# Kernel tuning notes

Hardware: AMD Instinct MI355X
Metric: run time of the kernel (lower is better)

The kernel has to match this reference:

```python
import jax, jax.numpy as jnp
import numpy as np

B, N, M, K = 8, 8192, 512, 32
C_IN, EMB = 3, 256
RADIUS2 = 0.1 * 0.1
EPS = 1e-5


def setup_inputs() -> dict:
    key = jax.random.key(0)
    ks = jax.random.split(key, 8)
    p = jax.random.uniform(ks[0], (B, N, 3), dtype=jnp.float32)           # coords in [0,1]^3
    x = jax.random.normal(ks[1], (B, C_IN, N), dtype=jnp.float32)          # features [B,C,N]
    def w(k, co, ci):
        return jax.random.normal(k, (co, ci), dtype=jnp.float32) / np.float32(np.sqrt(ci))
    return {
        "p": p, "x": x,
        # conv1: (6->256, BN+ReLU), (256->256, plain+bias)
        "W0": w(ks[2], EMB, 6), "g0": jnp.ones((EMB,), jnp.float32), "be0": jnp.zeros((EMB,), jnp.float32),
        "W1": w(ks[3], EMB, EMB), "b1": jnp.zeros((EMB,), jnp.float32),
        # conv2 (input doubled to 512): (512->512, BN+ReLU), (512->256, plain+bias)
        "W2": w(ks[4], 2 * EMB, 2 * EMB), "g2": jnp.ones((2 * EMB,), jnp.float32), "be2": jnp.zeros((2 * EMB,), jnp.float32),
        "W3": w(ks[5], EMB, 2 * EMB), "b3": jnp.zeros((EMB,), jnp.float32),
    }


def furthest_point_sample(p, m):
    # p: [B,N,3] -> idx [B,m] int32; starts at index 0 (matches CUDA FPS)
    b, n, _ = p.shape
    def step(carry, _):
        min_d, last = carry
        last_pt = jnp.take_along_axis(p, last[:, None, None], axis=1)     # [B,1,3]
        d = jnp.sum((p - last_pt) ** 2, axis=-1)                           # [B,N]
        min_d = jnp.minimum(min_d, d)
        nxt = jnp.argmax(min_d, axis=-1).astype(jnp.int32)
        return (min_d, nxt), last
    init = (jnp.full((b, n), 1e10, p.dtype), jnp.zeros((b,), jnp.int32))
    _, idx = jax.lax.scan(step, init, None, length=m)
    return idx.T                                                           # [B,m]


def ball_query(center_p, p, k, r2):
    # first-k-in-order points within radius; pad with first valid (center is always valid)
    d2 = jnp.sum((center_p[:, :, None, :] - p[:, None, :, :]) ** 2, axis=-1)  # [B,M,N]
    n = p.shape[1]
    keyv = jnp.where(d2 < r2, jnp.arange(n, dtype=jnp.int32), jnp.int32(n))   # [B,M,N]
    keys = jnp.sort(keyv, axis=-1)[..., :k]                                    # [B,M,K]
    valid = keys < n
    idx = jnp.where(valid, keys, keys[..., 0:1])
    return idx.astype(jnp.int32)


def bn_relu(f, g, b):
    # training-mode BatchNorm2d over (B, M, K) per channel, then ReLU
    mu = jnp.mean(f, axis=(0, 2, 3), keepdims=True)
    var = jnp.var(f, axis=(0, 2, 3), keepdims=True)
    fh = (f - mu) * jax.lax.rsqrt(var + EPS)
    return jax.nn.relu(fh * g[None, :, None, None] + b[None, :, None, None])


def reference(p, x, W0, g0, be0, W1, b1, W2, g2, be2, W3, b3):
    idx = furthest_point_sample(p, M)                                       # [B,M]
    center_p = jnp.take_along_axis(p, idx[:, :, None], axis=1)              # [B,M,3]
    gidx = ball_query(center_p, p, K, RADIUS2)                              # [B,M,K]
    grouped_xyz = jax.vmap(lambda pts, ix: pts[ix])(p, gidx)                # [B,M,K,3]
    dp = jnp.transpose(grouped_xyz - center_p[:, :, None, :], (0, 3, 1, 2))  # [B,3,M,K]
    fj = jax.vmap(lambda ft, ix: ft[:, ix])(x, gidx)                        # [B,C,M,K]
    center_x = jnp.take_along_axis(x, idx[:, None, :], axis=2)              # [B,C,M]
    f = jnp.concatenate([dp, fj - center_x[..., None]], axis=1)             # [B,6,M,K]  (dp_df)
    # conv1
    f = bn_relu(jnp.einsum('oc,bcmk->bomk', W0, f), g0, be0)
    f = jnp.einsum('oc,bcmk->bomk', W1, f) + b1[None, :, None, None]
    # mid max-pool concat
    fmax = jnp.max(f, axis=-1, keepdims=True)
    f = jnp.concatenate([jnp.broadcast_to(fmax, f.shape), f], axis=1)       # [B,512,M,K]
    # conv2
    f = bn_relu(jnp.einsum('oc,bcmk->bomk', W2, f), g2, be2)
    f = jnp.einsum('oc,bcmk->bomk', W3, f) + b3[None, :, None, None]
    out_f = jnp.max(f, axis=-1)                                             # [B,256,M]
    return (p, center_p, x, out_f)
```

## Files before the change

kernel.cpp:

```cpp
#include <hip/hip_runtime.h>

typedef unsigned short u16;
typedef unsigned int u32;
typedef unsigned long long u64;
typedef __bf16 bf16x8 __attribute__((ext_vector_type(8)));
typedef float v4f32 __attribute__((ext_vector_type(4)));

#define NP 8192
#define NM 512
#define LTOT 131072
#define NBM 4096
#define R2F 0.009999999776482582f

__device__ __forceinline__ float bf2f(u16 u) { return __uint_as_float(((u32)u) << 16); }
__device__ __forceinline__ u16 f2bf(float f) {
  u32 u = __float_as_uint(f);
  return (u16)((u + 0x7fffu + ((u >> 16) & 1u)) >> 16);
}
__device__ __forceinline__ void gl16(const void* g, void* l) {
  __builtin_amdgcn_global_load_lds((const __attribute__((address_space(1))) u32*)g,
                                   (__attribute__((address_space(3))) u32*)l, 16, 0, 0);
}

#define MFMA_COMPUTE() do { \
  bf16x8 a_[4], b_[4]; \
  _Pragma("unroll") \
  for (int mi_ = 0; mi_ < 4; ++mi_) a_[mi_] = *(const bf16x8*)&As[(wrow + mi_*16 + l15)*32 + l4*8]; \
  _Pragma("unroll") \
  for (int ni_ = 0; ni_ < 4; ++ni_) b_[ni_] = *(const bf16x8*)&Bs[(wcol + ni_*16 + l15)*32 + l4*8]; \
  _Pragma("unroll") \
  for (int mi_ = 0; mi_ < 4; ++mi_) { \
    _Pragma("unroll") \
    for (int ni_ = 0; ni_ < 4; ++ni_) \
      acc[mi_][ni_] = __builtin_amdgcn_mfma_f32_16x16x32_bf16(a_[mi_], b_[ni_], acc[mi_][ni_], 0, 0, 0); \
  } \
} while (0)

__global__ __launch_bounds__(1024) void k_fps_prep(
    const float* __restrict__ p, const float* __restrict__ x,
    const float* __restrict__ W1, const float* __restrict__ W2, const float* __restrict__ W3,
    float* __restrict__ outP, float* __restrict__ outC, float* __restrict__ outX,
    u16* __restrict__ w1b, u16* __restrict__ w2b, u16* __restrict__ w3b,
    float* __restrict__ statz, int* __restrict__ idxb)
{
  const int tid = threadIdx.x;
  if (blockIdx.x >= 8) {
    for (size_t i = (size_t)(blockIdx.x - 8) * 1024 + tid; i < 855040; i += 104 * 1024) {
      if (i < 196608)      outP[i] = p[i];
      else if (i < 393216) outX[i - 196608] = x[i - 196608];
      else if (i < 458752) w1b[i - 393216] = f2bf(W1[i - 393216]);
      else if (i < 720896) w2b[i - 458752] = f2bf(W2[i - 458752]);
      else if (i < 851968) w3b[i - 720896] = f2bf(W3[i - 720896]);
      else                 statz[i - 851968] = 0.0f;
    }
    return;
  }
  const int b = blockIdx.x;
  const float* pb = p + (size_t)b * NP * 3;
  __shared__ float pl[NP * 3];
  __shared__ u64 slot[3];
  float px[8], py[8], pz[8], md[8];
  u32 nj[8];
  #pragma unroll
  for (int q = 0; q < 8; ++q) {
    int j = tid + (q << 10);
    float a0 = pb[j*3+0], a1 = pb[j*3+1], a2 = pb[j*3+2];
    px[q] = a0; py[q] = a1; pz[q] = a2; md[q] = 1e10f;
    nj[q] = ~(u32)j;
    pl[j*3+0] = a0; pl[j*3+1] = a1; pl[j*3+2] = a2;
  }
  if (tid < 3) slot[tid] = 0ull;
  __syncthreads();
  int last = 0;
  float* ctr = outC + (size_t)b * NM * 3;
  int* ip = idxb + b * NM;
  for (int s = 0; s < NM; ++s) {
    const int sl = s % 3;
    float lx = pl[last*3], ly = pl[last*3+1], lz = pl[last*3+2];
    if (tid == 0) {
      ip[s] = last; ctr[s*3] = lx; ctr[s*3+1] = ly; ctr[s*3+2] = lz;
      slot[(s+1) % 3] = 0ull;
    }
    u64 bk = 0;
    #pragma unroll
    for (int q = 0; q < 8; ++q) {
      float dx = __fsub_rn(px[q], lx), dy = __fsub_rn(py[q], ly), dz = __fsub_rn(pz[q], lz);
      float d = __fadd_rn(__fadd_rn(__fmul_rn(dx,dx), __fmul_rn(dy,dy)), __fmul_rn(dz,dz));
      float nm = fminf(md[q], d);
      md[q] = nm;
      u64 key = ((u64)__float_as_uint(nm) << 32) | (u64)nj[q];
      bk = key > bk ? key : bk;
    }
    #pragma unroll
    for (int off = 1; off < 64; off <<= 1) {
      u64 o = __shfl_xor(bk, off);
      if (o > bk) bk = o;
    }
    if ((tid & 63) == 0)
      __hip_atomic_fetch_max(&slot[sl], bk, __ATOMIC_RELAXED, __HIP_MEMORY_SCOPE_WORKGROUP);
    __syncthreads();
    last = (int)(~(u32)(slot[sl] & 0xffffffffull));
  }
}

__global__ __launch_bounds__(256) void k_group(
    const float* __restrict__ p, const float* __restrict__ x,
    const float* __restrict__ ctr, const int* __restrict__ idxb,
    u16* __restrict__ f0)
{
  const int tid = threadIdx.x, wv = tid >> 6, lane = tid & 63;
  const int cm = blockIdx.x * 4 + wv;
  const int b = cm >> 9;
  __shared__ int selS[4][33];
  volatile int* sel = selS[wv];
  const float cx0 = ctr[cm*3+0], cy0 = ctr[cm*3+1], cz0 = ctr[cm*3+2];
  const float* pb = p + (size_t)b * NP * 3;
  int cnt = 0;
  for (int ch = 0; ch < NP/64; ++ch) {
    if (cnt >= 32) break;
    int j = (ch << 6) + lane;
    float qx = pb[j*3], qy = pb[j*3+1], qz = pb[j*3+2];
    float dx = __fsub_rn(cx0,qx), dy = __fsub_rn(cy0,qy), dz = __fsub_rn(cz0,qz);
    float d2 = __fadd_rn(__fadd_rn(__fmul_rn(dx,dx),__fmul_rn(dy,dy)),__fmul_rn(dz,dz));
    bool pr = d2 < R2F;
    u64 msk = __ballot(pr);
    int pos = cnt + (int)__popcll(msk & ((1ull << lane) - 1ull));
    if (pr && pos < 32) sel[pos] = j;
    cnt += (int)__popcll(msk);
  }
  if (lane < 32) {
    int jj = (lane < cnt) ? sel[lane] : sel[0];
    const float* xb = x + (size_t)b * 3 * NP;
    int ic = idxb[cm];
    float gx = pb[jj*3], gy = pb[jj*3+1], gz = pb[jj*3+2];
    size_t col = (size_t)cm * 32 + lane;
    f0[0*(size_t)LTOT + col] = f2bf(gx - cx0);
    f0[1*(size_t)LTOT + col] = f2bf(gy - cy0);
    f0[2*(size_t)LTOT + col] = f2bf(gz - cz0);
    f0[3*(size_t)LTOT + col] = f2bf(xb[jj]      - xb[ic]);
    f0[4*(size_t)LTOT + col] = f2bf(xb[NP+jj]   - xb[NP+ic]);
    f0[5*(size_t)LTOT + col] = f2bf(xb[2*NP+jj] - xb[2*NP+ic]);
  }
}

__global__ __launch_bounds__(256) void k_g1(
    const u16* __restrict__ f0, const float* __restrict__ W0, u16* __restrict__ h1)
{
  __shared__ float w0l[1536];
  const int tid = threadIdx.x;
  for (int i = tid; i < 1536; i += 256) w0l[i] = W0[i];
  __syncthreads();
  const size_t col = (size_t)blockIdx.x * 256 + tid;
  float fin[6];
  #pragma unroll
  for (int c = 0; c < 6; ++c) fin[c] = bf2f(f0[(size_t)c * LTOT + col]);
  #pragma unroll
  for (int ob = 0; ob < 8; ++ob) {
    u32 w[16];
    #pragma unroll
    for (int pr2 = 0; pr2 < 16; ++pr2) {
      float v0 = 0.f, v1 = 0.f;
      int o0 = ob*32 + pr2*2;
      #pragma unroll
      for (int c = 0; c < 6; ++c) {
        v0 = fmaf(w0l[o0*6 + c], fin[c], v0);
        v1 = fmaf(w0l[(o0+1)*6 + c], fin[c], v1);
      }
      w[pr2] = (u32)f2bf(v0) | ((u32)f2bf(v1) << 16);
    }
    uint4* dst = (uint4*)(h1 + ((size_t)ob * LTOT + col) * 32);
    #pragma unroll
    for (int t4 = 0; t4 < 4; ++t4)
      dst[t4] = make_uint4(w[t4*4], w[t4*4+1], w[t4*4+2], w[t4*4+3]);
  }
}

__global__ __launch_bounds__(256) void k_stat(
    const u16* __restrict__ hb, float* __restrict__ sums, float* __restrict__ sqs)
{
  const int tid = threadIdx.x;
  const int cb = blockIdx.x >> 5, cc = blockIdx.x & 31;
  const int slot = tid & 3, cl = tid >> 2;
  float s[8], q[8];
  #pragma unroll
  for (int j = 0; j < 8; ++j) { s[j] = 0.f; q[j] = 0.f; }
  const u16* base = hb + (size_t)cb * LTOT * 32;
  for (int i = 0; i < 64; ++i) {
    size_t col = (size_t)cc * 4096 + i * 64 + cl;
    uint4 v = *(const uint4*)(base + col * 32 + slot * 8);
    u32 qa[4] = {v.x, v.y, v.z, v.w};
    #pragma unroll
    for (int t2 = 0; t2 < 4; ++t2) {
      float lo = bf2f((u16)(qa[t2] & 0xffffu));
      float hi = bf2f((u16)(qa[t2] >> 16));
      s[2*t2]   += lo; q[2*t2]   = fmaf(lo, lo, q[2*t2]);
      s[2*t2+1] += hi; q[2*t2+1] = fmaf(hi, hi, q[2*t2+1]);
    }
  }
  __shared__ float ls[32], lq[32];
  if (tid < 32) { ls[tid] = 0.f; lq[tid] = 0.f; }
  __syncthreads();
  #pragma unroll
  for (int j = 0; j < 8; ++j) {
    atomicAdd(&ls[slot*8 + j], s[j]);
    atomicAdd(&lq[slot*8 + j], q[j]);
  }
  __syncthreads();
  if (tid < 32) {
    atomicAdd(&sums[cb*32 + tid], ls[tid]);
    atomicAdd(&sqs[cb*32 + tid], lq[tid]);
  }
}

__global__ void k_fin(const float* __restrict__ sums, const float* __restrict__ sqs,
                      const float* __restrict__ g, const float* __restrict__ be,
                      float* __restrict__ S, float* __restrict__ T, int C)
{
  int t = threadIdx.x;
  if (t < C) {
    const float inv = 1.0f / 131072.0f;
    float mu = sums[t] * inv;
    float var = sqs[t] * inv - mu * mu;
    float s = g[t] / sqrtf(var + 1e-5f);
    S[t] = s; T[t] = be[t] - mu * s;
  }
}

__device__ __forceinline__ void xf_store(u16* Bs, int idx, uint4 q, int cb,
                                         const float* sS, const float* sT)
{
  u32 w[4]; u32 qa[4] = {q.x, q.y, q.z, q.w};
  #pragma unroll
  for (int t2 = 0; t2 < 4; ++t2) {
    float a  = fmaxf(fmaf(sS[cb + 2*t2],     bf2f((u16)(qa[t2] & 0xffffu)), sT[cb + 2*t2]), 0.f);
    float bv = fmaxf(fmaf(sS[cb + 2*t2 + 1], bf2f((u16)(qa[t2] >> 16)),     sT[cb + 2*t2 + 1]), 0.f);
    w[t2] = (u32)f2bf(a) | ((u32)f2bf(bv) << 16);
  }
  *(uint4*)&Bs[idx * 8] = make_uint4(w[0], w[1], w[2], w[3]);
}

__global__ __launch_bounds__(256) void k_gemm2(
    const u16* __restrict__ wA, const u16* __restrict__ hin,
    const float* __restrict__ Sc, const float* __restrict__ Tc,
    const float* __restrict__ bias,
    u16* __restrict__ h2, u16* __restrict__ fmaxb)
{
  __shared__ alignas(16) u16 As[4096];
  __shared__ alignas(16) u16 Bs[4096];
  __shared__ float sS[256], sT[256];
  const int tid = threadIdx.x;
  sS[tid] = Sc[tid]; sT[tid] = Tc[tid];
  const int oT = blockIdx.x & 1, cT = blockIdx.x >> 1;
  const int lane = tid & 63, wv = tid >> 6;
  const int wrow = (wv >> 1) * 64, wcol = (wv & 1) * 64;
  const int l15 = lane & 15, l4 = lane >> 4;
  v4f32 acc[4][4];
  #pragma unroll
  for (int mi = 0; mi < 4; ++mi)
    #pragma unroll
    for (int ni = 0; ni < 4; ++ni) acc[mi][ni] = (v4f32){0.f,0.f,0.f,0.f};
  const int idx0 = tid, idx1 = 256 + tid;
  const int r0 = idx0 >> 2, sg0 = idx0 & 3, r1 = idx1 >> 2, sg1 = idx1 & 3;
  __syncthreads();
  for (int kt = 0; kt < 8; ++kt) {
    const size_t bb = (size_t)kt * LTOT + (size_t)cT * 128;
    uint4 q0 = *(const uint4*)(hin + (bb + r0) * 32 + sg0 * 8);
    uint4 q1 = *(const uint4*)(hin + (bb + r1) * 32 + sg1 * 8);
    if (kt) __syncthreads();
    gl16(wA + (size_t)(oT*128 + r0) * 256 + kt*32 + sg0*8, &As[idx0 * 8]);
    gl16(wA + (size_t)(oT*128 + r1) * 256 + kt*32 + sg1*8, &As[idx1 * 8]);
    xf_store(Bs, idx0, q0, kt*32 + sg0*8, sS, sT);
    xf_store(Bs, idx1, q1, kt*32 + sg1*8, sS, sT);
    asm volatile("s_waitcnt vmcnt(0)" ::: "memory");
    __syncthreads();
    MFMA_COMPUTE();
  }
  const int oB = oT*128 + wrow + l4*4;
  const int cB = cT*128 + wcol + l15;
  #pragma unroll
  for (int mi = 0; mi < 4; ++mi) {
    const float4 bv = *(const float4*)&bias[oB + mi*16];
    #pragma unroll
    for (int ni = 0; ni < 4; ++ni) {
      acc[mi][ni][0] += bv.x; acc[mi][ni][1] += bv.y;
      acc[mi][ni][2] += bv.z; acc[mi][ni][3] += bv.w;
    }
  }
  #pragma unroll
  for (int mi = 0; mi < 4; ++mi) {
    const int o = oB + mi*16;
    const size_t rb = (size_t)(o >> 5) * LTOT * 32 + (o & 31);
    #pragma unroll
    for (int ni = 0; ni < 4; ++ni) {
      ushort4 u; u.x = f2bf(acc[mi][ni][0]); u.y = f2bf(acc[mi][ni][1]);
      u.z = f2bf(acc[mi][ni][2]); u.w = f2bf(acc[mi][ni][3]);
      *(ushort4*)&h2[rb + (size_t)(cB + ni*16) * 32] = u;
    }
  }
  #pragma unroll
  for (int g = 0; g < 2; ++g) {
    const int bm = (cT*128 + wcol + g*32) >> 5;
    #pragma unroll
    for (int mi = 0; mi < 4; ++mi) {
      float a0 = fmaxf(acc[mi][2*g][0], acc[mi][2*g+1][0]);
      float a1 = fmaxf(acc[mi][2*g][1], acc[mi][2*g+1][1]);
      float a2 = fmaxf(acc[mi][2*g][2], acc[mi][2*g+1][2]);
      float a3 = fmaxf(acc[mi][2*g][3], acc[mi][2*g+1][3]);
      #pragma unroll
      for (int off = 1; off < 16; off <<= 1) {
        a0 = fmaxf(a0, __shfl_xor(a0, off));
        a1 = fmaxf(a1, __shfl_xor(a1, off));
        a2 = fmaxf(a2, __shfl_xor(a2, off));
        a3 = fmaxf(a3, __shfl_xor(a3, off));
      }
      if (l15 == 0) {
        const int o = oB + mi*16;
        ushort4 u; u.x=f2bf(a0); u.y=f2bf(a1); u.z=f2bf(a2); u.w=f2bf(a3);
        *(ushort4*)&fmaxb[((size_t)(o >> 5) * NBM + bm) * 32 + (o & 31)] = u;
      }
    }
  }
}

__global__ __launch_bounds__(256) void k_fmb(
    const u16* __restrict__ wA, const u16* __restrict__ fmaxb, float* __restrict__ fmb)
{
  __shared__ alignas(16) u16 As[4096];
  __shared__ alignas(16) u16 Bs[4096];
  const int tid = threadIdx.x;
  const int oT = blockIdx.x & 3, cT = blockIdx.x >> 2;
  const int lane = tid & 63, wv = tid >> 6;
  const int wrow = (wv >> 1) * 64, wcol = (wv & 1) * 64;
  const int l15 = lane & 15, l4 = lane >> 4;
  v4f32 acc[4][4];
  #pragma unroll
  for (int mi = 0; mi < 4; ++mi)
    #pragma unroll
    for (int ni = 0; ni < 4; ++ni) acc[mi][ni] = (v4f32){0.f,0.f,0.f,0.f};
  const int idx0 = tid, idx1 = 256 + tid;
  const int r0 = idx0 >> 2, sg0 = idx0 & 3, r1 = idx1 >> 2, sg1 = idx1 & 3;
  for (int kt = 0; kt < 8; ++kt) {
    if (kt) __syncthreads();
    gl16(wA + (size_t)(oT*128 + r0) * 512 + kt*32 + sg0*8, &As[idx0 * 8]);
    gl16(wA + (size_t)(oT*128 + r1) * 512 + kt*32 + sg1*8, &As[idx1 * 8]);
    const size_t bb = (size_t)kt * NBM + (size_t)cT * 128;
    gl16(fmaxb + (bb + r0) * 32 + sg0 * 8, &Bs[idx0 * 8]);
    gl16(fmaxb + (bb + r1) * 32 + sg1 * 8, &Bs[idx1 * 8]);
    asm volatile("s_waitcnt vmcnt(0)" ::: "memory");
    __syncthreads();
    MFMA_COMPUTE();
  }
  const int oB = oT*128 + wrow + l4*4;
  const int cB = cT*128 + wcol + l15;
  #pragma unroll
  for (int mi = 0; mi < 4; ++mi) {
    const int o = oB + mi*16;
    #pragma unroll
    for (int ni = 0; ni < 4; ++ni) {
      const int colg = cB + ni*16;
      fmb[(size_t)(o+0)*NBM + colg] = acc[mi][ni][0];
      fmb[(size_t)(o+1)*NBM + colg] = acc[mi][ni][1];
      fmb[(size_t)(o+2)*NBM + colg] = acc[mi][ni][2];
      fmb[(size_t)(o+3)*NBM + colg] = acc[mi][ni][3];
    }
  }
}

__global__ __launch_bounds__(256) void k_gemm3(
    const u16* __restrict__ wA, const u16* __restrict__ hin,
    const float* __restrict__ fmb, u16* __restrict__ h3)
{
  __shared__ alignas(16) u16 As[4096];
  __shared__ alignas(16) u16 Bs[4096];
  const int tid = threadIdx.x;
  const int oT = blockIdx.x & 3, cT = blockIdx.x >> 2;
  const int lane = tid & 63, wv = tid >> 6;
  const int wrow = (wv >> 1) * 64, wcol = (wv & 1) * 64;
  const int l15 = lane & 15, l4 = lane >> 4;
  v4f32 acc[4][4];
  #pragma unroll
  for (int mi = 0; mi < 4; ++mi)
    #pragma unroll
    for (int ni = 0; ni < 4; ++ni) acc[mi][ni] = (v4f32){0.f,0.f,0.f,0.f};
  const int idx0 = tid, idx1 = 256 + tid;
  const int r0 = idx0 >> 2, sg0 = idx0 & 3, r1 = idx1 >> 2, sg1 = idx1 & 3;
  for (int kt = 0; kt < 8; ++kt) {
    if (kt) __syncthreads();
    gl16(wA + (size_t)(oT*128 + r0) * 512 + 256 + kt*32 + sg0*8, &As[idx0 * 8]);
    gl16(wA + (size_t)(oT*128 + r1) * 512 + 256 + kt*32 + sg1*8, &As[idx1 * 8]);
    const size_t bb = (size_t)kt * LTOT + (size_t)cT * 128;
    gl16(hin + (bb + r0) * 32 + sg0 * 8, &Bs[idx0 * 8]);
    gl16(hin + (bb + r1) * 32 + sg1 * 8, &Bs[idx1 * 8]);
    asm volatile("s_waitcnt vmcnt(0)" ::: "memory");
    __syncthreads();
    MFMA_COMPUTE();
  }
  const int oB = oT*128 + wrow + l4*4;
  const int cB = cT*128 + wcol + l15;
  #pragma unroll
  for (int mi = 0; mi < 4; ++mi) {
    const int o = oB + mi*16;
    const size_t rb = (size_t)(o >> 5) * LTOT * 32 + (o & 31);
    #pragma unroll
    for (int hf = 0; hf < 2; ++hf) {
      const int bm = (cT*128 + wcol + hf*32) >> 5;
      float e0 = fmb[(size_t)(o+0)*NBM + bm];
      float e1 = fmb[(size_t)(o+1)*NBM + bm];
      float e2 = fmb[(size_t)(o+2)*NBM + bm];
      float e3 = fmb[(size_t)(o+3)*NBM + bm];
      #pragma unroll
      for (int nn = 0; nn < 2; ++nn) {
        const int ni = hf*2 + nn;
        ushort4 u;
        u.x = f2bf(acc[mi][ni][0] + e0);
        u.y = f2bf(acc[mi][ni][1] + e1);
        u.z = f2bf(acc[mi][ni][2] + e2);
        u.w = f2bf(acc[mi][ni][3] + e3);
        *(ushort4*)&h3[rb + (size_t)(cB + ni*16) * 32] = u;
      }
    }
  }
}

__global__ __launch_bounds__(256) void k_gemm4(
    const u16* __restrict__ wA, const u16* __restrict__ hin,
    const float* __restrict__ Sc, const float* __restrict__ Tc,
    const float* __restrict__ bias, float* __restrict__ outF)
{
  __shared__ alignas(16) u16 As[4096];
  __shared__ alignas(16) u16 Bs[4096];
  __shared__ float sS[512], sT[512];
  const int tid = threadIdx.x;
  sS[tid] = Sc[tid]; sT[tid] = Tc[tid];
  sS[tid+256] = Sc[tid+256]; sT[tid+256] = Tc[tid+256];
  const int oT = blockIdx.x & 1, cT = blockIdx.x >> 1;
  const int lane = tid & 63, wv = tid >> 6;
  const int wrow = (wv >> 1) * 64, wcol = (wv & 1) * 64;
  const int l15 = lane & 15, l4 = lane >> 4;
  v4f32 acc[4][4];
  #pragma unroll
  for (int mi = 0; mi < 4; ++mi)
    #pragma unroll
    for (int ni = 0; ni < 4; ++ni) acc[mi][ni] = (v4f32){0.f,0.f,0.f,0.f};
  const int idx0 = tid, idx1 = 256 + tid;
  const int r0 = idx0 >> 2, sg0 = idx0 & 3, r1 = idx1 >> 2, sg1 = idx1 & 3;
  __syncthreads();
  for (int kt = 0; kt < 16; ++kt) {
    const size_t bb = (size_t)kt * LTOT + (size_t)cT * 128;
    uint4 q0 = *(const uint4*)(hin + (bb + r0) * 32 + sg0 * 8);
    uint4 q1 = *(const uint4*)(hin + (bb + r1) * 32 + sg1 * 8);
    if (kt) __syncthreads();
    gl16(wA + (size_t)(oT*128 + r0) * 512 + kt*32 + sg0*8, &As[idx0 * 8]);
    gl16(wA + (size_t)(oT*128 + r1) * 512 + kt*32 + sg1*8, &As[idx1 * 8]);
    xf_store(Bs, idx0, q0, kt*32 + sg0*8, sS, sT);
    xf_store(Bs, idx1, q1, kt*32 + sg1*8, sS, sT);
    asm volatile("s_waitcnt vmcnt(0)" ::: "memory");
    __syncthreads();
    MFMA_COMPUTE();
  }
  const int oB = oT*128 + wrow + l4*4;
  #pragma unroll
  for (int mi = 0; mi < 4; ++mi) {
    const float4 bv = *(const float4*)&bias[oB + mi*16];
    #pragma unroll
    for (int ni = 0; ni < 4; ++ni) {
      acc[mi][ni][0] += bv.x; acc[mi][ni][1] += bv.y;
      acc[mi][ni][2] += bv.z; acc[mi][ni][3] += bv.w;
    }
  }
  #pragma unroll
  for (int g = 0; g < 2; ++g) {
    const int bm = (cT*128 + wcol + g*32) >> 5;
    const int bI = bm >> 9, mm = bm & 511;
    #pragma unroll
    for (int mi = 0; mi < 4; ++mi) {
      float a0 = fmaxf(acc[mi][2*g][0], acc[mi][2*g+1][0]);
      float a1 = fmaxf(acc[mi][2*g][1], acc[mi][2*g+1][1]);
      float a2 = fmaxf(acc[mi][2*g][2], acc[mi][2*g+1][2]);
      float a3 = fmaxf(acc[mi][2*g][3], acc[mi][2*g+1][3]);
      #pragma unroll
      for (int off = 1; off < 16; off <<= 1) {
        a0 = fmaxf(a0, __shfl_xor(a0, off));
        a1 = fmaxf(a1, __shfl_xor(a1, off));
        a2 = fmaxf(a2, __shfl_xor(a2, off));
        a3 = fmaxf(a3, __shfl_xor(a3, off));
      }
      if (l15 == 0) {
        const int o = oB + mi*16;
        outF[((size_t)bI*256 + o+0)*512 + mm] = a0;
        outF[((size_t)bI*256 + o+1)*512 + mm] = a1;
        outF[((size_t)bI*256 + o+2)*512 + mm] = a2;
        outF[((size_t)bI*256 + o+3)*512 + mm] = a3;
      }
    }
  }
}

extern "C" void kernel_launch(void* const* d_in, const int* in_sizes, int n_in,
                              void* d_out, int out_size, void* d_ws, size_t ws_size,
                              hipStream_t stream)
{
  (void)in_sizes; (void)n_in; (void)out_size; (void)ws_size;
  const float* p   = (const float*)d_in[0];
  const float* x   = (const float*)d_in[1];
  const float* W0  = (const float*)d_in[2];
  const float* g0  = (const float*)d_in[3];
  const float* be0 = (const float*)d_in[4];
  const float* W1  = (const float*)d_in[5];
  const float* b1  = (const float*)d_in[6];
  const float* W2  = (const float*)d_in[7];
  const float* g2  = (const float*)d_in[8];
  const float* be2 = (const float*)d_in[9];
  const float* W3  = (const float*)d_in[10];
  const float* b3  = (const float*)d_in[11];
  float* out  = (float*)d_out;
  float* outP = out;
  float* outC = out + 196608;
  float* outX = out + 208896;
  float* outF = out + 405504;
  char* ws = (char*)d_ws;
  u16* h2    = (u16*)(ws);
  u16* h3    = (u16*)(ws + 67108864);
  u16* h1    = h3;
  u16* f0    = (u16*)(ws + 201326592);
  u16* fmaxb = (u16*)(ws + 202899456);
  float* fmb = (float*)(ws + 204996608);
  u16* w1b   = (u16*)(ws + 213385216);
  u16* w2b   = (u16*)(ws + 213516288);
  u16* w3b   = (u16*)(ws + 214040576);
  int* idxb  = (int*)(ws + 214302720);
  float* statz = (float*)(ws + 214319104);
  float* sum1 = statz;        float* sq1 = statz + 256;
  float* sum2 = statz + 512;  float* sq2 = statz + 1024;
  float* s0 = statz + 1536;   float* t0 = statz + 1792;
  float* s2 = statz + 2048;   float* t2 = statz + 2560;

  k_fps_prep<<<112, 1024, 0, stream>>>(p, x, W1, W2, W3, outP, outC, outX,
                                       w1b, w2b, w3b, statz, idxb);
  k_group<<<1024, 256, 0, stream>>>(p, x, outC, idxb, f0);
  k_g1<<<512, 256, 0, stream>>>(f0, W0, h1);
  k_stat<<<256, 256, 0, stream>>>(h1, sum1, sq1);
  k_fin<<<1, 512, 0, stream>>>(sum1, sq1, g0, be0, s0, t0, 256);
  k_gemm2<<<2048, 256, 0, stream>>>(w1b, h1, s0, t0, b1, h2, fmaxb);
  k_fmb<<<128, 256, 0, stream>>>(w2b, fmaxb, fmb);
  k_gemm3<<<4096, 256, 0, stream>>>(w2b, h2, fmb, h3);
  k_stat<<<512, 256, 0, stream>>>(h3, sum2, sq2);
  k_fin<<<1, 512, 0, stream>>>(sum2, sq2, g2, be2, s2, t2, 512);
  k_gemm4<<<2048, 256, 0, stream>>>(w3b, h3, s2, t2, b3, outF);
}
```

Baseline: 905.9 us.

## Speed up FPS argmax with packed fp32 math and DPP float max plus ballot

The sequential furthest-point-sampling loop now computes distances with packed v_pk_add/v_pk_mul fp32 instructions, two points per instruction. The per-step argmax no longer runs a 64-bit key shuffle reduction. It does a 32-bit float max through DPP row/bcast steps, reads lane 63, and recovers the smallest matching index with ballots and ctz. This cuts the latency of the 512 serial steps, which bound the FPS block. It relies on float max equality and ballot ordering to keep the smallest-index tie-break, and replacing rounded fsub with adding a negated value keeps the arithmetic bit-exact.

```diff
diff --git a/kernel.cpp b/kernel.cpp
--- a/kernel.cpp
+++ b/kernel.cpp
@@ -5,6 +5,7 @@
 typedef unsigned long long u64;
 typedef __bf16 bf16x8 __attribute__((ext_vector_type(8)));
 typedef float v4f32 __attribute__((ext_vector_type(4)));
+typedef float f32x2 __attribute__((ext_vector_type(2)));
 
 #define NP 8192
 #define NM 512
@@ -20,6 +21,27 @@
 __device__ __forceinline__ void gl16(const void* g, void* l) {
   __builtin_amdgcn_global_load_lds((const __attribute__((address_space(1))) u32*)g,
                                    (__attribute__((address_space(3))) u32*)l, 16, 0, 0);
+}
+
+__device__ __forceinline__ f32x2 pk_add(f32x2 a, f32x2 b) {
+  f32x2 r; asm("v_pk_add_f32 %0, %1, %2" : "=v"(r) : "v"(a), "v"(b)); return r;
+}
+__device__ __forceinline__ f32x2 pk_mul(f32x2 a, f32x2 b) {
+  f32x2 r; asm("v_pk_mul_f32 %0, %1, %2" : "=v"(r) : "v"(a), "v"(b)); return r;
+}
+
+__device__ __forceinline__ float wave_fmax_dpp63(float v) {
+#define FSTEP(CTRL) { \
+    u32 o_ = (u32)__builtin_amdgcn_update_dpp(0, (int)__float_as_uint(v), CTRL, 0xF, 0xF, true); \
+    v = fmaxf(v, __uint_as_float(o_)); }
+  FSTEP(0x111)
+  FSTEP(0x112)
+  FSTEP(0x114)
+  FSTEP(0x118)
+  FSTEP(0x142)
+  FSTEP(0x143)
+#undef FSTEP
+  return v;
 }
 
 #define MFMA_COMPUTE() do { \
@@ -59,17 +81,17 @@
   const float* pb = p + (size_t)b * NP * 3;
   __shared__ float pl[NP * 3];
   __shared__ u64 slot[3];
-  float px[8], py[8], pz[8], md[8];
-  u32 nj[8];
+  f32x2 pxv[4], pyv[4], pzv[4];
+  float md[8];
   #pragma unroll
   for (int q = 0; q < 8; ++q) {
     int j = tid + (q << 10);
     float a0 = pb[j*3+0], a1 = pb[j*3+1], a2 = pb[j*3+2];
-    px[q] = a0; py[q] = a1; pz[q] = a2; md[q] = 1e10f;
-    nj[q] = ~(u32)j;
+    pxv[q>>1][q&1] = a0; pyv[q>>1][q&1] = a1; pzv[q>>1][q&1] = a2; md[q] = 1e10f;
     pl[j*3+0] = a0; pl[j*3+1] = a1; pl[j*3+2] = a2;
   }
   if (tid < 3) slot[tid] = 0ull;
+  const u32 wbase = (u32)__builtin_amdgcn_readfirstlane(tid & 0x3C0);
   __syncthreads();
   int last = 0;
   float* ctr = outC + (size_t)b * NM * 3;
@@ -81,23 +103,31 @@
       ip[s] = last; ctr[s*3] = lx; ctr[s*3+1] = ly; ctr[s*3+2] = lz;
       slot[(s+1) % 3] = 0ull;
     }
-    u64 bk = 0;
-    #pragma unroll
-    for (int q = 0; q < 8; ++q) {
-      float dx = __fsub_rn(px[q], lx), dy = __fsub_rn(py[q], ly), dz = __fsub_rn(pz[q], lz);
-      float d = __fadd_rn(__fadd_rn(__fmul_rn(dx,dx), __fmul_rn(dy,dy)), __fmul_rn(dz,dz));
-      float nm = fminf(md[q], d);
-      md[q] = nm;
-      u64 key = ((u64)__float_as_uint(nm) << 32) | (u64)nj[q];
-      bk = key > bk ? key : bk;
-    }
-    #pragma unroll
-    for (int off = 1; off < 64; off <<= 1) {
-      u64 o = __shfl_xor(bk, off);
-      if (o > bk) bk = o;
+    const f32x2 nlx = {-lx, -lx}, nly = {-ly, -ly}, nlz = {-lz, -lz};
+    #pragma unroll
+    for (int h = 0; h < 4; ++h) {
+      f32x2 dx = pk_add(pxv[h], nlx);
+      f32x2 dy = pk_add(pyv[h], nly);
+      f32x2 dz = pk_add(pzv[h], nlz);
+      f32x2 d2 = pk_add(pk_add(pk_mul(dx,dx), pk_mul(dy,dy)), pk_mul(dz,dz));
+      md[2*h]   = fminf(md[2*h],   d2.x);
+      md[2*h+1] = fminf(md[2*h+1], d2.y);
+    }
+    float t01 = fmaxf(md[0], md[1]), t23 = fmaxf(md[2], md[3]);
+    float t45 = fmaxf(md[4], md[5]), t67 = fmaxf(md[6], md[7]);
+    float wmx = fmaxf(fmaxf(t01, t23), fmaxf(t45, t67));
+    wmx = wave_fmax_dpp63(wmx);
+    u32 wmb = (u32)__builtin_amdgcn_readlane((int)__float_as_uint(wmx), 63);
+    float wm = __uint_as_float(wmb);
+    u32 jq = 0;
+    #pragma unroll
+    for (int q = 7; q >= 0; --q) {
+      u64 mq = __ballot(md[q] == wm);
+      if (mq) jq = (u32)__builtin_ctzll(mq) + (u32)(q << 10);
     }
     if ((tid & 63) == 0)
-      __hip_atomic_fetch_max(&slot[sl], bk, __ATOMIC_RELAXED, __HIP_MEMORY_SCOPE_WORKGROUP);
+      __hip_atomic_fetch_max(&slot[sl], ((u64)wmb << 32) | (u64)(~(wbase + jq)),
+                             __ATOMIC_RELAXED, __HIP_MEMORY_SCOPE_WORKGROUP);
     __syncthreads();
     last = (int)(~(u32)(slot[sl] & 0xffffffffull));
   }
```

After: 817.6 us. 9.7% less time.

## Derive first BN stats from input covariance, fuse second BN stats into GEMM epilogue

Applied to the files above, without the earlier changes.

The first BatchNorm statistics now come from a 6-channel input moment matrix (first and second moments), which k_fin1 projects through W0 analytically. This replaces the pass over the 256-channel h1 buffer. The second BN's sum and sum-of-squares are accumulated inside the k_gemm3 epilogue with wave shuffles and global atomics, which removes the separate k_stat read of h3. The trade-offs: the stats are taken from fp32 values rather than bf16-rounded ones, the covariance form can lose precision through cancellation, and the GEMM epilogue now issues many atomics.

```diff
diff --git a/kernel.cpp b/kernel.cpp
--- a/kernel.cpp
+++ b/kernel.cpp
@@ -143,6 +143,78 @@
   }
 }
 
+__global__ __launch_bounds__(256) void k_cov(const u16* __restrict__ f0, float* __restrict__ cov)
+{
+  const int tid = threadIdx.x;
+  const size_t col = (size_t)blockIdx.x * 256 + tid;
+  float f[6];
+  #pragma unroll
+  for (int c = 0; c < 6; ++c) f[c] = bf2f(f0[(size_t)c * LTOT + col]);
+  float v[27];
+  int n = 0;
+  #pragma unroll
+  for (int c = 0; c < 6; ++c) v[n++] = f[c];
+  #pragma unroll
+  for (int i = 0; i < 6; ++i)
+    #pragma unroll
+    for (int j = i; j < 6; ++j) v[n++] = f[i] * f[j];
+  #pragma unroll
+  for (int k = 0; k < 27; ++k) {
+    float s = v[k];
+    #pragma unroll
+    for (int off = 1; off < 64; off <<= 1) s += __shfl_xor(s, off);
+    v[k] = s;
+  }
+  __shared__ float ls[27];
+  if (tid < 27) ls[tid] = 0.f;
+  __syncthreads();
+  if ((tid & 63) == 0) {
+    #pragma unroll
+    for (int k = 0; k < 27; ++k) atomicAdd(&ls[k], v[k]);
+  }
+  __syncthreads();
+  if (tid < 27) atomicAdd(&cov[tid], ls[tid]);
+}
+
+__global__ void k_fin1(const float* __restrict__ cov, const float* __restrict__ W0,
+                       const float* __restrict__ g, const float* __restrict__ be,
+                       float* __restrict__ S, float* __restrict__ T)
+{
+  int c = threadIdx.x;
+  const float inv = 1.0f / 131072.0f;
+  float w[6];
+  #pragma unroll
+  for (int k = 0; k < 6; ++k) w[k] = W0[c*6 + k];
+  float mu = 0.f;
+  #pragma unroll
+  for (int k = 0; k < 6; ++k) mu = fmaf(w[k], cov[k], mu);
+  mu *= inv;
+  float e2 = 0.f;
+  int n = 6;
+  #pragma unroll
+  for (int i = 0; i < 6; ++i)
+    #pragma unroll
+    for (int j = i; j < 6; ++j) {
+      float coeff = (i == j) ? w[i]*w[j] : 2.f*w[i]*w[j];
+      e2 = fmaf(coeff, cov[n++] * inv, e2);
+    }
+  float var = e2 - mu * mu;
+  float s = g[c] / sqrtf(var + 1e-5f);
+  S[c] = s; T[c] = be[c] - mu * s;
+}
+
+__global__ void k_fin2(const float* __restrict__ sums, const float* __restrict__ sqs,
+                       const float* __restrict__ g, const float* __restrict__ be,
+                       float* __restrict__ S, float* __restrict__ T)
+{
+  int t = threadIdx.x;
+  const float inv = 1.0f / 131072.0f;
+  float mu = sums[t] * inv;
+  float var = sqs[t] * inv - mu * mu;
+  float s = g[t] / sqrtf(var + 1e-5f);
+  S[t] = s; T[t] = be[t] - mu * s;
+}
+
 __global__ __launch_bounds__(256) void k_g1(
     const u16* __restrict__ f0, const float* __restrict__ W0, u16* __restrict__ h1)
 {
@@ -172,57 +244,6 @@
     #pragma unroll
     for (int t4 = 0; t4 < 4; ++t4)
       dst[t4] = make_uint4(w[t4*4], w[t4*4+1], w[t4*4+2], w[t4*4+3]);
-  }
-}
-
-__global__ __launch_bounds__(256) void k_stat(
-    const u16* __restrict__ hb, float* __restrict__ sums, float* __restrict__ sqs)
-{
-  const int tid = threadIdx.x;
-  const int cb = blockIdx.x >> 5, cc = blockIdx.x & 31;
-  const int slot = tid & 3, cl = tid >> 2;
-  float s[8], q[8];
-  #pragma unroll
-  for (int j = 0; j < 8; ++j) { s[j] = 0.f; q[j] = 0.f; }
-  const u16* base = hb + (size_t)cb * LTOT * 32;
-  for (int i = 0; i < 64; ++i) {
-    size_t col = (size_t)cc * 4096 + i * 64 + cl;
-    uint4 v = *(const uint4*)(base + col * 32 + slot * 8);
-    u32 qa[4] = {v.x, v.y, v.z, v.w};
-    #pragma unroll
-    for (int t2 = 0; t2 < 4; ++t2) {
-      float lo = bf2f((u16)(qa[t2] & 0xffffu));
-      float hi = bf2f((u16)(qa[t2] >> 16));
-      s[2*t2]   += lo; q[2*t2]   = fmaf(lo, lo, q[2*t2]);
-      s[2*t2+1] += hi; q[2*t2+1] = fmaf(hi, hi, q[2*t2+1]);
-    }
-  }
-  __shared__ float ls[32], lq[32];
-  if (tid < 32) { ls[tid] = 0.f; lq[tid] = 0.f; }
-  __syncthreads();
-  #pragma unroll
-  for (int j = 0; j < 8; ++j) {
-    atomicAdd(&ls[slot*8 + j], s[j]);
-    atomicAdd(&lq[slot*8 + j], q[j]);
-  }
-  __syncthreads();
-  if (tid < 32) {
-    atomicAdd(&sums[cb*32 + tid], ls[tid]);
-    atomicAdd(&sqs[cb*32 + tid], lq[tid]);
-  }
-}
-
-__global__ void k_fin(const float* __restrict__ sums, const float* __restrict__ sqs,
-                      const float* __restrict__ g, const float* __restrict__ be,
-                      float* __restrict__ S, float* __restrict__ T, int C)
-{
-  int t = threadIdx.x;
-  if (t < C) {
-    const float inv = 1.0f / 131072.0f;
-    float mu = sums[t] * inv;
-    float var = sqs[t] * inv - mu * mu;
-    float s = g[t] / sqrtf(var + 1e-5f);
-    S[t] = s; T[t] = be[t] - mu * s;
   }
 }
 
@@ -368,7 +389,8 @@
 
 __global__ __launch_bounds__(256) void k_gemm3(
     const u16* __restrict__ wA, const u16* __restrict__ hin,
-    const float* __restrict__ fmb, u16* __restrict__ h3)
+    const float* __restrict__ fmb, u16* __restrict__ h3,
+    float* __restrict__ stS, float* __restrict__ stQ)
 {
   __shared__ alignas(16) u16 As[4096];
   __shared__ alignas(16) u16 Bs[4096];
@@ -401,6 +423,7 @@
   for (int mi = 0; mi < 4; ++mi) {
     const int o = oB + mi*16;
     const size_t rb = (size_t)(o >> 5) * LTOT * 32 + (o & 31);
+    float st[4] = {0.f,0.f,0.f,0.f}, sq[4] = {0.f,0.f,0.f,0.f};
     #pragma unroll
     for (int hf = 0; hf < 2; ++hf) {
       const int bm = (cT*128 + wcol + hf*32) >> 5;
@@ -411,12 +434,30 @@
       #pragma unroll
       for (int nn = 0; nn < 2; ++nn) {
         const int ni = hf*2 + nn;
+        float v0 = acc[mi][ni][0] + e0;
+        float v1 = acc[mi][ni][1] + e1;
+        float v2 = acc[mi][ni][2] + e2;
+        float v3 = acc[mi][ni][3] + e3;
+        st[0] += v0; sq[0] = fmaf(v0, v0, sq[0]);
+        st[1] += v1; sq[1] = fmaf(v1, v1, sq[1]);
+        st[2] += v2; sq[2] = fmaf(v2, v2, sq[2]);
+        st[3] += v3; sq[3] = fmaf(v3, v3, sq[3]);
         ushort4 u;
-        u.x = f2bf(acc[mi][ni][0] + e0);
-        u.y = f2bf(acc[mi][ni][1] + e1);
-        u.z = f2bf(acc[mi][ni][2] + e2);
-        u.w = f2bf(acc[mi][ni][3] + e3);
+        u.x = f2bf(v0); u.y = f2bf(v1); u.z = f2bf(v2); u.w = f2bf(v3);
         *(ushort4*)&h3[rb + (size_t)(cB + ni*16) * 32] = u;
+      }
+    }
+    #pragma unroll
+    for (int e = 0; e < 4; ++e) {
+      float s = st[e], q = sq[e];
+      #pragma unroll
+      for (int off = 1; off < 16; off <<= 1) {
+        s += __shfl_xor(s, off);
+        q += __shfl_xor(q, off);
+      }
+      if (l15 == 0) {
+        atomicAdd(&stS[o + e], s);
+        atomicAdd(&stQ[o + e], q);
       }
     }
   }
@@ -530,21 +571,21 @@
   u16* w3b   = (u16*)(ws + 214040576);
   int* idxb  = (int*)(ws + 214302720);
   float* statz = (float*)(ws + 214319104);
-  float* sum1 = statz;        float* sq1 = statz + 256;
-  float* sum2 = statz + 512;  float* sq2 = statz + 1024;
+  float* cov  = statz;
+  float* sum2 = statz + 512;
+  float* sq2  = statz + 1024;
   float* s0 = statz + 1536;   float* t0 = statz + 1792;
   float* s2 = statz + 2048;   float* t2 = statz + 2560;
 
   k_fps_prep<<<112, 1024, 0, stream>>>(p, x, W1, W2, W3, outP, outC, outX,
                                        w1b, w2b, w3b, statz, idxb);
   k_group<<<1024, 256, 0, stream>>>(p, x, outC, idxb, f0);
+  k_cov<<<512, 256, 0, stream>>>(f0, cov);
+  k_fin1<<<1, 256, 0, stream>>>(cov, W0, g0, be0, s0, t0);
   k_g1<<<512, 256, 0, stream>>>(f0, W0, h1);
-  k_stat<<<256, 256, 0, stream>>>(h1, sum1, sq1);
-  k_fin<<<1, 512, 0, stream>>>(sum1, sq1, g0, be0, s0, t0, 256);
   k_gemm2<<<2048, 256, 0, stream>>>(w1b, h1, s0, t0, b1, h2, fmaxb);
   k_fmb<<<128, 256, 0, stream>>>(w2b, fmaxb, fmb);
-  k_gemm3<<<4096, 256, 0, stream>>>(w2b, h2, fmb, h3);
-  k_stat<<<512, 256, 0, stream>>>(h3, sum2, sq2);
-  k_fin<<<1, 512, 0, stream>>>(sum2, sq2, g2, be2, s2, t2, 512);
+  k_gemm3<<<4096, 256, 0, stream>>>(w2b, h2, fmb, h3, sum2, sq2);
+  k_fin2<<<1, 512, 0, stream>>>(sum2, sq2, g2, be2, s2, t2);
   k_gemm4<<<2048, 256, 0, stream>>>(w3b, h3, s2, t2, b3, outF);
 }
```

Measured after the change: 1.037 ms. 14.5% more time.
